# Optimization experiments

Hardware: AMD Instinct MI355X
Metric: run time of the kernel (lower is better)

## Reference

```python
import jax, jax.numpy as jnp
import numpy as np

B, T, F, H = 4096, 8, 64, 64          # batch(=edges), time windows, feat_dim, attention hidden
N, De = 2048, 128                      # graph nodes, node/edge feature dim
NF, NC = 64, 2                         # conv filters, num classes
HID1, HID2 = 256, 24                   # LazyLinear dims
FLAT = NF * T * 2 * F                  # flattened conv output


def setup_inputs() -> dict:
    key = jax.random.key(0)
    ks = jax.random.split(key, 25)
    rn = lambda k, shape, s=0.05: jax.random.normal(k, shape, jnp.float32) * s
    return {
        "X_nume": jax.random.normal(ks[0], (B, T, F), jnp.float32),
        "src": jax.random.randint(ks[1], (B,), 0, N, jnp.int32),
        "dst": jax.random.randint(ks[2], (B,), 0, N, jnp.int32),
        "node_feat": jax.random.normal(ks[3], (N, De), jnp.float32),
        "edge_feat": jax.random.normal(ks[4], (B, De), jnp.float32),
        # attention params (original uses uniform(0,1); scaled uniform here)
        "attn_W": jax.random.uniform(ks[5], (F, H), jnp.float32) * 0.1,
        "attn_U": jax.random.uniform(ks[6], (F, H), jnp.float32) * 0.1,
        "attn_V": jax.random.uniform(ks[7], (H, 1), jnp.float32) * 0.1,
        # conv
        "conv_w": rn(ks[8], (NF, 1, 2, 2)), "conv_b": rn(ks[9], (NF,)),
        # GraphConv 1/2 (weights stored [in, out])
        "gc1_W": rn(ks[10], (De, 128)), "gc1_b": rn(ks[11], (128,)),
        "gc2_W": rn(ks[12], (128, 8)), "gc2_b": rn(ks[13], (8,)),
        # edge linears
        "lin1_W": rn(ks[14], (De, 128)), "lin1_b": rn(ks[15], (128,)),
        "lin2_W": rn(ks[16], (128, 8)), "lin2_b": rn(ks[17], (8,)),
        # MLP head
        "fc1_W": rn(ks[18], (FLAT, HID1), 0.01), "fc1_b": rn(ks[19], (HID1,)),
        "fc2_W": rn(ks[20], (HID1, HID2)), "fc2_b": rn(ks[21], (HID2,)),
        "fc3_W": rn(ks[22], (HID2 + 24, NC)), "fc3_b": rn(ks[23], (NC,)),
    }


def _graph_conv(h, W, b, src, dst, n):
    # DGL GraphConv, norm='both': out = D_in^{-1/2} A D_out^{-1/2} h W + b
    ones = jnp.ones(src.shape[0], h.dtype)
    deg_out = jnp.clip(jax.ops.segment_sum(ones, src, num_segments=n), 1.0)
    deg_in = jnp.clip(jax.ops.segment_sum(ones, dst, num_segments=n), 1.0)
    hs = h * jax.lax.rsqrt(deg_out)[:, None]
    agg = jax.ops.segment_sum(hs[src], dst, num_segments=n)  # [N, in]
    agg = agg * jax.lax.rsqrt(deg_in)[:, None]
    return agg @ W + b


def _forward(X_nume, src, dst, node_feat, edge_feat,
             attn_W, attn_U, attn_V, conv_w, conv_b,
             gc1_W, gc1_b, gc2_W, gc2_b, lin1_W, lin1_b, lin2_W, lin2_b,
             fc1_W, fc1_b, fc2_W, fc2_b, fc3_W, fc3_b):
    # ---- temporal attention (vectorized O(T^2)) ----
    a = jnp.einsum('btf,fh->bth', X_nume, attn_W)   # x_i W
    u = jnp.einsum('btf,fh->bth', X_nume, attn_U)   # x_j U
    # e[b,i,j] = tanh(a_i + u_j) @ V  -> [B,T,T]
    e = jnp.einsum('bijh,h->bij', jnp.tanh(a[:, :, None, :] + u[:, None, :, :]), attn_V[:, 0])
    alpha = jax.nn.softmax(e, axis=2)
    # c_i = sum_{j != i} alpha_ij x_j  (softmax over all j, self term excluded from sum)
    ctx = jnp.einsum('bij,bjf->bif', alpha, X_nume)
    diag = jnp.diagonal(alpha, axis1=1, axis2=2)    # [B,T]
    ctx = ctx - diag[:, :, None] * X_nume
    att_out = jnp.concatenate([X_nume, ctx], axis=-1)  # [B,T,2F]

    # ---- CNN ----
    conv_in = att_out[:, None, :, :]  # [B,1,T,2F]
    conv_out = jax.lax.conv_general_dilated(
        conv_in, conv_w, window_strides=(1, 1), padding='SAME',
        dimension_numbers=('NCHW', 'OIHW', 'NCHW')) + conv_b[None, :, None, None]
    conv_out = jax.nn.relu(conv_out)  # [B,NF,T,2F]

    # ---- dual GraphConv message passing ----
    h1 = jax.nn.relu(_graph_conv(node_feat, gc1_W, gc1_b, src, dst, N))
    e1 = jax.nn.relu(edge_feat @ lin1_W + lin1_b)
    h2 = _graph_conv(h1, gc2_W, gc2_b, src, dst, N)   # no relu (matches source)
    e2 = jax.nn.relu(e1 @ lin2_W + lin2_b)
    edge_x = h2[src] + h2[dst] + e2                    # [E,8]
    node_feats = jnp.stack([h2[src], h2[dst], edge_x], axis=1).reshape(B, -1)  # [B,24]

    # ---- MLP head ----
    out = conv_out.reshape(B, -1)
    out = jax.nn.relu(out @ fc1_W + fc1_b)
    out = jax.nn.relu(out @ fc2_W + fc2_b)
    out = jnp.concatenate([out, node_feats], axis=1)
    return out @ fc3_W + fc3_b  # [B, NC]


def reference(X_nume, src, dst, node_feat, edge_feat,
              attn_W, attn_U, attn_V, conv_w, conv_b,
              gc1_W, gc1_b, gc2_W, gc2_b, lin1_W, lin1_b, lin2_W, lin2_b,
              fc1_W, fc1_b, fc2_W, fc2_b, fc3_W, fc3_b):
    return _forward(X_nume, src, dst, node_feat, edge_feat,
                    attn_W, attn_U, attn_V, conv_w, conv_b,
                    gc1_W, gc1_b, gc2_W, gc2_b, lin1_W, lin1_b, lin2_W, lin2_b,
                    fc1_W, fc1_b, fc2_W, fc2_b, fc3_W, fc3_b)
```

## Files before the change

### kernel.cpp

```cpp
#include <hip/hip_runtime.h>
#include <stdint.h>
#include <stddef.h>

typedef float    f32x4  __attribute__((ext_vector_type(4)));
typedef short    bf16x8 __attribute__((ext_vector_type(8)));
typedef uint16_t u16x8  __attribute__((ext_vector_type(8)));
typedef uint32_t u32x4  __attribute__((ext_vector_type(4)));

#define ATT_ROW 136

__device__ __forceinline__ uint16_t f2bf(float x) {
  union { float f; uint32_t u; } c; c.f = x;
  return (uint16_t)((c.u + 0x7FFFu + ((c.u >> 16) & 1u)) >> 16);
}
__device__ __forceinline__ float bf2f(uint16_t h) {
  union { uint32_t u; float f; } c; c.u = ((uint32_t)h) << 16;
  return c.f;
}
__device__ __forceinline__ int S64s(int a) { return a ^ (((a >> 6) & 7) << 4); }

__device__ __forceinline__ void cp16(void* lds, const void* g) {
  __builtin_amdgcn_global_load_lds((const __attribute__((address_space(1))) void*)g,
                                   (__attribute__((address_space(3))) void*)lds, 16, 0, 0);
}
__device__ __forceinline__ float fast_tanh(float t) {
  float r = __expf(-2.f * t);
  return 1.f - 2.f * r / (1.f + r);
}

__global__ __launch_bounds__(256) void k_prep(const float* __restrict__ W1,
                                              uint16_t* __restrict__ W1s) {
  __shared__ float st[32 * 256];
  const int c = blockIdx.x, tid = threadIdx.x;
  const float* src = W1 + (size_t)c * 32 * 256;
#pragma unroll
  for (int it = 0; it < 8; ++it) {
    int u = it * 256 + tid;
    ((f32x4*)st)[u] = ((const f32x4*)src)[u];
  }
  __syncthreads();
  uint16_t* dstc = W1s + (size_t)c * 8192;
#pragma unroll
  for (int q = 0; q < 4; ++q) {
    int p  = q * 256 + tid;
    int Np = p >> 2, Gp = p & 3;
    int n  = Np ^ ((Np >> 2) & 1);
    int g  = Gp ^ (n & 3);
    uint32_t w[4];
#pragma unroll
    for (int e2 = 0; e2 < 4; ++e2) {
      uint16_t lo = f2bf(st[(g * 8 + 2 * e2) * 256 + n]);
      uint16_t hi = f2bf(st[(g * 8 + 2 * e2 + 1) * 256 + n]);
      w[e2] = (uint32_t)lo | ((uint32_t)hi << 16);
    }
    u32x4 v; v.x = w[0]; v.y = w[1]; v.z = w[2]; v.w = w[3];
    *(u32x4*)(dstc + (size_t)p * 8) = v;
  }
}

__global__ __launch_bounds__(512) void k_att(const float* __restrict__ X,
    const float* __restrict__ aW, const float* __restrict__ aU,
    const float* __restrict__ aV, uint16_t* __restrict__ att) {
  __shared__ float sa[8][8][66];
  __shared__ float su[8][8][66];
  __shared__ float sal[8][64];
  __shared__ float sv[64];
  const int tid = threadIdx.x, lane = tid & 63, w = tid >> 6;
  if (tid < 64) sv[tid] = aV[tid];
  __syncthreads();
  for (int rep = 0; rep < 2; ++rep) {
    int b  = blockIdx.x * 16 + w * 2 + rep;
    int bu = __builtin_amdgcn_readfirstlane(b);
    const float* xb = X + (size_t)bu * 512;
    float xi[8];
#pragma unroll
    for (int i = 0; i < 8; ++i) xi[i] = xb[i * 64 + lane];
    float a[8], u[8];
#pragma unroll
    for (int i = 0; i < 8; ++i) { a[i] = 0.f; u[i] = 0.f; }
#pragma unroll
    for (int f = 0; f < 64; ++f) {
      float wf = aW[f * 64 + lane];
      float uf = aU[f * 64 + lane];
#pragma unroll
      for (int i = 0; i < 8; ++i) {
        float xs = xb[i * 64 + f];
        a[i] = fmaf(xs, wf, a[i]);
        u[i] = fmaf(xs, uf, u[i]);
      }
    }
#pragma unroll
    for (int i = 0; i < 8; ++i) { sa[w][i][lane] = a[i]; su[w][i][lane] = u[i]; }
    __syncthreads();
    int i2 = lane >> 3, j2 = lane & 7;
    float ev = 0.f;
#pragma unroll
    for (int h = 0; h < 64; ++h)
      ev = fmaf(fast_tanh(sa[w][i2][h] + su[w][j2][h]), sv[h], ev);
    float m = ev;
    m = fmaxf(m, __shfl_xor(m, 1));
    m = fmaxf(m, __shfl_xor(m, 2));
    m = fmaxf(m, __shfl_xor(m, 4));
    float p = __expf(ev - m);
    float s = p;
    s += __shfl_xor(s, 1); s += __shfl_xor(s, 2); s += __shfl_xor(s, 4);
    sal[w][lane] = p / s;
    __syncthreads();
#pragma unroll
    for (int i = 0; i < 8; ++i) {
      float c = 0.f;
#pragma unroll
      for (int j = 0; j < 8; ++j) c = fmaf(sal[w][i * 8 + j], xi[j], c);
      c = fmaf(-sal[w][i * 8 + i], xi[i], c);
      size_t ro = ((size_t)b * 9 + i) * ATT_ROW;
      att[ro + lane]      = f2bf(xi[i]);
      att[ro + 64 + lane] = f2bf(c);
      if (lane < 8) att[ro + 128 + lane] = 0;
    }
    {
      size_t ro = ((size_t)b * 9 + 8) * ATT_ROW;
      att[ro + lane] = 0; att[ro + 64 + lane] = 0;
      if (lane < 8) att[ro + 128 + lane] = 0;
    }
    __syncthreads();
  }
}

__global__ void k_deg(const int* __restrict__ src, const int* __restrict__ dst,
                      float* degO, float* degI) {
  int t = blockIdx.x * 256 + threadIdx.x;
  if (t < 4096) {
    atomicAdd(degO + src[t], 1.f);
    atomicAdd(degI + dst[t], 1.f);
  }
}
__global__ __launch_bounds__(256) void k_gca(const float* __restrict__ h,
    const int* __restrict__ src, const int* __restrict__ dst,
    const float* __restrict__ degO, float* __restrict__ agg) {
  int t = blockIdx.x * 256 + threadIdx.x;
  int e = t >> 7, d = t & 127;
  int s = src[e];
  float sc = rsqrtf(fmaxf(degO[s], 1.f));
  atomicAdd(agg + (size_t)dst[e] * 128 + d, h[(size_t)s * 128 + d] * sc);
}
__global__ __launch_bounds__(128) void k_gc1b(const float* __restrict__ agg,
    const float* __restrict__ degI, const float* __restrict__ Wt,
    const float* __restrict__ bs, float* __restrict__ h1) {
  __shared__ float vs[128];
  int n = blockIdx.x, t = threadIdx.x;
  float sc = rsqrtf(fmaxf(degI[n], 1.f));
  vs[t] = agg[(size_t)n * 128 + t] * sc;
  __syncthreads();
  float acc = bs[t];
#pragma unroll 8
  for (int d = 0; d < 128; ++d) acc = fmaf(vs[d], Wt[d * 128 + t], acc);
  h1[(size_t)n * 128 + t] = fmaxf(acc, 0.f);
}
__global__ __launch_bounds__(128) void k_gc2b(const float* __restrict__ agg,
    const float* __restrict__ degI, const float* __restrict__ Wt,
    const float* __restrict__ bs, float* __restrict__ h2) {
  __shared__ float vs[128];
  int n = blockIdx.x, t = threadIdx.x;
  float sc = rsqrtf(fmaxf(degI[n], 1.f));
  vs[t] = agg[(size_t)n * 128 + t] * sc;
  __syncthreads();
  if (t < 8) {
    float acc = bs[t];
#pragma unroll 8
    for (int d = 0; d < 128; ++d) acc = fmaf(vs[d], Wt[d * 8 + t], acc);
    h2[(size_t)n * 8 + t] = acc;
  }
}
__global__ __launch_bounds__(128) void k_e12(const float* __restrict__ ef,
    const float* __restrict__ W1, const float* __restrict__ b1,
    const float* __restrict__ W2, const float* __restrict__ b2,
    float* __restrict__ e2) {
  __shared__ float efs[128];
  __shared__ float t1s[128];
  int t = threadIdx.x;
  for (int it = 0; it < 16; ++it) {
    int b = blockIdx.x * 16 + it;
    efs[t] = ef[(size_t)b * 128 + t];
    __syncthreads();
    float acc = b1[t];
#pragma unroll 8
    for (int d = 0; d < 128; ++d) acc = fmaf(efs[d], W1[d * 128 + t], acc);
    t1s[t] = fmaxf(acc, 0.f);
    __syncthreads();
    if (t < 8) {
      float a2 = b2[t];
#pragma unroll 8
      for (int h = 0; h < 128; ++h) a2 = fmaf(t1s[h], W2[h * 8 + t], a2);
      e2[(size_t)b * 8 + t] = fmaxf(a2, 0.f);
    }
    __syncthreads();
  }
}

#define NS 64
struct Win { u16x8 a0, b0; uint16_t ae, be; };

__global__ __launch_bounds__(512, 4) void k_gemm(const uint16_t* __restrict__ W1s,
    const uint16_t* __restrict__ att, const float* __restrict__ conv_w,
    const float* __restrict__ conv_b, float* __restrict__ out1) {
  __shared__ __align__(16) char smem[49152];
  char* Abuf = smem;
  char* Bbuf = smem + 16384;

  const int tid = threadIdx.x;
  const int lane = tid & 63, ln15 = lane & 15, g = lane >> 4;
  const int wid = tid >> 6, wm = wid >> 2, wn = wid & 3;
  const int bid = blockIdx.x;
  const int i_row = bid & 7, oh = (bid >> 3) & 1, jh = (bid >> 4) & 1;
  const int btile = bid >> 5;
  const int b0 = btile * 128;
  const int am = tid >> 2, ag = tid & 3;

  f32x4 acc[4][4];
#pragma unroll
  for (int mt = 0; mt < 4; ++mt)
#pragma unroll
    for (int nt = 0; nt < 4; ++nt) { f32x4 z = {0.f, 0.f, 0.f, 0.f}; acc[mt][nt] = z; }

  auto loadWin = [&](int ss) {
    int jg = jh * 2 + (ss & 1);
    int j0 = jg * 32 + ag * 8;
    const uint16_t* r0 = att + ((size_t)(b0 + am) * 9 + i_row) * ATT_ROW + j0;
    const uint16_t* r1 = r0 + ATT_ROW;
    Win w;
    w.a0 = *(const u16x8*)r0; w.ae = r0[8];
    w.b0 = *(const u16x8*)r1; w.be = r1[8];
    return w;
  };

  auto computeA = [&](const Win& w, int ss, char* Ab) {
    float t0[9], t1[9];
#pragma unroll
    for (int e = 0; e < 8; ++e) {
      t0[e] = bf2f((uint16_t)w.a0[e]);
      t1[e] = bf2f((uint16_t)w.b0[e]);
    }
    t0[8] = bf2f(w.ae); t1[8] = bf2f(w.be);
    int o = oh * 32 + (ss >> 1);
    float c0  = conv_b[o];
    float k00 = conv_w[o * 4 + 0], k01 = conv_w[o * 4 + 1];
    float k10 = conv_w[o * 4 + 2], k11 = conv_w[o * 4 + 3];
    uint32_t pk[4];
#pragma unroll
    for (int e2 = 0; e2 < 8; e2 += 2) {
      float v0 = fmaf(k00, t0[e2],     fmaf(k01, t0[e2 + 1], fmaf(k10, t1[e2],     fmaf(k11, t1[e2 + 1], c0))));
      float v1 = fmaf(k00, t0[e2 + 1], fmaf(k01, t0[e2 + 2], fmaf(k10, t1[e2 + 1], fmaf(k11, t1[e2 + 2], c0))));
      v0 = fmaxf(v0, 0.f); v1 = fmaxf(v1, 0.f);
      uint32_t pr;
      asm("v_cvt_pk_bf16_f32 %0, %1, %2" : "=v"(pr) : "v"(v0), "v"(v1));
      pk[e2 >> 1] = pr;
    }
    u32x4 wv; wv.x = pk[0]; wv.y = pk[1]; wv.z = pk[2]; wv.w = pk[3];
    *(u32x4*)(Ab + S64s(am * 64 + ag * 16)) = wv;
  };

  auto stageB = [&](int ss, char* Bb) {
    int jg = jh * 2 + (ss & 1);
    int c = (oh * 32 + (ss >> 1)) * 32 + i_row * 4 + jg;
    const char* gsrc = (const char*)W1s + (size_t)c * 16384;
#pragma unroll
    for (int it = 0; it < 2; ++it) {
      char* ldsb = Bb + (size_t)(it * 512 + (tid & ~63)) * 16;
      cp16(ldsb, gsrc + (size_t)(it * 512 + tid) * 16);
    }
  };

  auto mfmaStep = [&](const char* Ab, const char* Bb) {
    bf16x8 bfr[4];
#pragma unroll
    for (int nt = 0; nt < 4; ++nt) {
      int n = wn * 64 + nt * 16 + ln15;
      bfr[nt] = *(const bf16x8*)(Bb + S64s(n * 64 + g * 16));
    }
    bf16x8 afr[4];
#pragma unroll
    for (int mt = 0; mt < 4; ++mt) {
      int m = wm * 64 + mt * 16 + ln15;
      afr[mt] = *(const bf16x8*)(Ab + S64s(m * 64 + g * 16));
    }
#pragma unroll
    for (int mt = 0; mt < 4; ++mt)
#pragma unroll
      for (int nt = 0; nt < 4; ++nt)
        acc[mt][nt] = __builtin_amdgcn_mfma_f32_16x16x32_bf16(afr[mt], bfr[nt], acc[mt][nt], 0, 0, 0);
  };

  Win wA = loadWin(0);
  computeA(wA, 0, Abuf);
  stageB(0, Bbuf);
  Win wB = loadWin(1);
  __syncthreads();

#pragma unroll 1
  for (int s2 = 0; s2 < NS; s2 += 2) {
    {
      const int ss = s2;
      if (ss + 1 < NS) stageB(ss + 1, Bbuf + 16384);
      if (ss + 2 < NS) wA = loadWin(ss + 2);
      if (ss + 1 < NS) computeA(wB, ss + 1, Abuf + 8192);
      mfmaStep(Abuf, Bbuf);
      __syncthreads();
    }
    {
      const int ss = s2 + 1;
      if (ss + 1 < NS) stageB(ss + 1, Bbuf);
      if (ss + 2 < NS) wB = loadWin(ss + 2);
      if (ss + 1 < NS) computeA(wA, ss + 1, Abuf);
      mfmaStep(Abuf + 8192, Bbuf + 16384);
      __syncthreads();
    }
  }

  const int rbase = b0 + wm * 64 + (lane >> 4) * 4;
  const int cbase = wn * 64 + ln15;
#pragma unroll
  for (int mt = 0; mt < 4; ++mt)
#pragma unroll
    for (int nt = 0; nt < 4; ++nt)
#pragma unroll
      for (int r = 0; r < 4; ++r)
        atomicAdd(out1 + (size_t)(rbase + mt * 16 + r) * 256 + cbase + nt * 16,
                  acc[mt][nt][r]);
}

__global__ __launch_bounds__(512) void k_fin(const float* __restrict__ out1,
    const float* __restrict__ fc1_b, const float* __restrict__ fc2_W,
    const float* __restrict__ fc2_b, const float* __restrict__ fc3_W,
    const float* __restrict__ fc3_b, const int* __restrict__ src,
    const int* __restrict__ dst, const float* __restrict__ h2,
    const float* __restrict__ e2, float* __restrict__ outp) {
  int lane = threadIdx.x & 63, w = threadIdx.x >> 6;
  int b  = blockIdx.x * 8 + w;
  int bu = __builtin_amdgcn_readfirstlane(b);
  f32x4 o4 = ((const f32x4*)(out1 + (size_t)bu * 256))[lane];
  f32x4 bi = ((const f32x4*)fc1_b)[lane];
  float v[4];
#pragma unroll
  for (int r = 0; r < 4; ++r) v[r] = fmaxf(o4[r] + bi[r], 0.f);
  float a24[24];
#pragma unroll
  for (int q = 0; q < 24; ++q) a24[q] = 0.f;
#pragma unroll
  for (int r = 0; r < 4; ++r) {
    const float* wr = fc2_W + (size_t)(lane * 4 + r) * 24;
#pragma unroll
    for (int q = 0; q < 24; ++q) a24[q] = fmaf(v[r], wr[q], a24[q]);
  }
#pragma unroll
  for (int q = 0; q < 24; ++q) {
    float t = a24[q];
    t += __shfl_xor(t, 1);  t += __shfl_xor(t, 2);  t += __shfl_xor(t, 4);
    t += __shfl_xor(t, 8);  t += __shfl_xor(t, 16); t += __shfl_xor(t, 32);
    a24[q] = fmaxf(t + fc2_b[q], 0.f);
  }
  int s = src[bu], d2 = dst[bu];
  float nf[24];
#pragma unroll
  for (int q = 0; q < 8; ++q) {
    float hs = h2[(size_t)s * 8 + q];
    float hd = h2[(size_t)d2 * 8 + q];
    nf[q] = hs; nf[8 + q] = hd; nf[16 + q] = hs + hd + e2[(size_t)bu * 8 + q];
  }
  if (lane == 0) {
#pragma unroll
    for (int c = 0; c < 2; ++c) {
      float r = fc3_b[c];
#pragma unroll
      for (int q = 0; q < 24; ++q) r = fmaf(a24[q], fc3_W[q * 2 + c], r);
#pragma unroll
      for (int q = 0; q < 24; ++q) r = fmaf(nf[q], fc3_W[(24 + q) * 2 + c], r);
      outp[(size_t)bu * 2 + c] = r;
    }
  }
}

extern "C" void kernel_launch(void* const* d_in, const int* in_sizes, int n_in,
                              void* d_out, int out_size, void* d_ws, size_t ws_size,
                              hipStream_t stream) {
  const float* X         = (const float*)d_in[0];
  const int*   src       = (const int*)d_in[1];
  const int*   dst       = (const int*)d_in[2];
  const float* node_feat = (const float*)d_in[3];
  const float* edge_feat = (const float*)d_in[4];
  const float* attn_W    = (const float*)d_in[5];
  const float* attn_U    = (const float*)d_in[6];
  const float* attn_V    = (const float*)d_in[7];
  const float* conv_w    = (const float*)d_in[8];
  const float* conv_b    = (const float*)d_in[9];
  const float* gc1_W     = (const float*)d_in[10];
  const float* gc1_b     = (const float*)d_in[11];
  const float* gc2_W     = (const float*)d_in[12];
  const float* gc2_b     = (const float*)d_in[13];
  const float* lin1_W    = (const float*)d_in[14];
  const float* lin1_b    = (const float*)d_in[15];
  const float* lin2_W    = (const float*)d_in[16];
  const float* lin2_b    = (const float*)d_in[17];
  const float* fc1_W     = (const float*)d_in[18];
  const float* fc1_b     = (const float*)d_in[19];
  const float* fc2_W     = (const float*)d_in[20];
  const float* fc2_b     = (const float*)d_in[21];
  const float* fc3_W     = (const float*)d_in[22];
  const float* fc3_b     = (const float*)d_in[23];

  char* ws = (char*)d_ws;
  float*    out1 = (float*)(ws + 0);
  float*    agg1 = (float*)(ws + 4194304);
  float*    agg2 = (float*)(ws + 5242880);
  float*    degO = (float*)(ws + 6291456);
  float*    degI = (float*)(ws + 6299648);
  uint16_t* W1s  = (uint16_t*)(ws + 6307840);
  uint16_t* att  = (uint16_t*)(ws + 39862272);
  float*    h1   = (float*)(ws + 49889280);
  float*    h2   = (float*)(ws + 50937856);
  float*    e2   = (float*)(ws + 51003392);

  hipMemsetAsync(d_ws, 0, 6307840, stream);

  k_prep<<<dim3(2048), dim3(256), 0, stream>>>(fc1_W, W1s);
  k_att <<<dim3(256),  dim3(512), 0, stream>>>(X, attn_W, attn_U, attn_V, att);
  k_deg <<<dim3(16),   dim3(256), 0, stream>>>(src, dst, degO, degI);
  k_gca <<<dim3(2048), dim3(256), 0, stream>>>(node_feat, src, dst, degO, agg1);
  k_gc1b<<<dim3(2048), dim3(128), 0, stream>>>(agg1, degI, gc1_W, gc1_b, h1);
  k_gca <<<dim3(2048), dim3(256), 0, stream>>>(h1, src, dst, degO, agg2);
  k_gc2b<<<dim3(2048), dim3(128), 0, stream>>>(agg2, degI, gc2_W, gc2_b, h2);
  k_e12 <<<dim3(256),  dim3(128), 0, stream>>>(edge_feat, lin1_W, lin1_b, lin2_W, lin2_b, e2);
  k_gemm<<<dim3(1024), dim3(512), 0, stream>>>(W1s, att, conv_w, conv_b, out1);
  k_fin <<<dim3(512),  dim3(512), 0, stream>>>(out1, fc1_b, fc2_W, fc2_b, fc3_W, fc3_b,
                                               src, dst, h2, e2, (float*)d_out);
}
```

Measured before the change: 558.9 us.

## Triple-buffer B tiles in k_gemm with partial vmcnt waits

Grows shared memory to hold three B-stage buffers and prefetches B two stages ahead, cycling through them modulo 3 while A stays double-buffered. The full __syncthreads is replaced by an explicit partial vmcnt wait plus s_barrier, so in-flight global-to-LDS loads for later stages are not drained every iteration. This is meant to hide global load latency behind MFMA work. The larger LDS footprint may cut the number of resident blocks per CU, and the hand-written vmcnt count is fragile if the number of issued loads changes.

After: 554.1 us. Within noise of the previous version (-0.9%).

```diff
diff --git a/kernel.cpp b/kernel.cpp
--- a/kernel.cpp
+++ b/kernel.cpp
@@ -203,7 +203,7 @@
 __global__ __launch_bounds__(512, 4) void k_gemm(const uint16_t* __restrict__ W1s,
     const uint16_t* __restrict__ att, const float* __restrict__ conv_w,
     const float* __restrict__ conv_b, float* __restrict__ out1) {
-  __shared__ __align__(16) char smem[49152];
+  __shared__ __align__(16) char smem[65536];
   char* Abuf = smem;
   char* Bbuf = smem + 16384;
 
@@ -290,30 +290,29 @@
         acc[mt][nt] = __builtin_amdgcn_mfma_f32_16x16x32_bf16(afr[mt], bfr[nt], acc[mt][nt], 0, 0, 0);
   };
 
-  Win wA = loadWin(0);
-  computeA(wA, 0, Abuf);
   stageB(0, Bbuf);
-  Win wB = loadWin(1);
-  __syncthreads();
+  stageB(1, Bbuf + 16384);
+  Win w0 = loadWin(0);
+  computeA(w0, 0, Abuf);
+  Win wc = loadWin(1);
+  asm volatile("s_waitcnt lgkmcnt(0)" ::: "memory");
+  __builtin_amdgcn_sched_barrier(0);
+  __builtin_amdgcn_s_barrier();
+  __builtin_amdgcn_sched_barrier(0);
 
 #pragma unroll 1
-  for (int s2 = 0; s2 < NS; s2 += 2) {
-    {
-      const int ss = s2;
-      if (ss + 1 < NS) stageB(ss + 1, Bbuf + 16384);
-      if (ss + 2 < NS) wA = loadWin(ss + 2);
-      if (ss + 1 < NS) computeA(wB, ss + 1, Abuf + 8192);
-      mfmaStep(Abuf, Bbuf);
-      __syncthreads();
-    }
-    {
-      const int ss = s2 + 1;
-      if (ss + 1 < NS) stageB(ss + 1, Bbuf);
-      if (ss + 2 < NS) wB = loadWin(ss + 2);
-      if (ss + 1 < NS) computeA(wA, ss + 1, Abuf);
-      mfmaStep(Abuf + 8192, Bbuf + 16384);
-      __syncthreads();
-    }
+  for (int ss = 0; ss < NS; ++ss) {
+    if (ss + 2 < NS) stageB(ss + 2, Bbuf + ((ss + 2) % 3) * 16384);
+    Win wn = wc;
+    if (ss + 2 < NS) wn = loadWin(ss + 2);
+    if (ss + 1 < NS) computeA(wc, ss + 1, Abuf + ((ss + 1) & 1) * 8192);
+    wc = wn;
+    mfmaStep(Abuf + (ss & 1) * 8192, Bbuf + (ss % 3) * 16384);
+    asm volatile("s_waitcnt vmcnt(6)" ::: "memory");
+    asm volatile("s_waitcnt lgkmcnt(0)" ::: "memory");
+    __builtin_amdgcn_sched_barrier(0);
+    __builtin_amdgcn_s_barrier();
+    __builtin_amdgcn_sched_barrier(0);
   }
 
   const int rbase = b0 + wm * 64 + (lane >> 4) * 4;
```
